# Kernel tuning notes

Hardware: AMD Instinct MI355X
Metric: run time of the kernel (lower is better)

The kernel has to match this reference:

```python
import jax, jax.numpy as jnp
import numpy as np

N_SRC, M, K, H = 100000, 20000, 32, 128
NEG_SLOPE = 0.01  # torch LeakyReLU default


def setup_inputs() -> dict:
    key = jax.random.key(0)
    ks = jax.random.split(key, 8)
    nei = jax.random.randint(ks[0], (M, K), 0, N_SRC)
    h = jax.random.normal(ks[1], (N_SRC, 1), dtype=jnp.float32)
    h_refer = jax.random.normal(ks[2], (M, 1), dtype=jnp.float32)
    # map_l / map_r: Linear(1, H), weight init U[0,1), bias U[0,0.01)
    map_l_w = jax.random.uniform(ks[3], (H, 1), dtype=jnp.float32)
    map_l_b = jax.random.uniform(ks[4], (H,), dtype=jnp.float32) * 0.01
    map_r_w = jax.random.uniform(ks[5], (H, 1), dtype=jnp.float32)
    map_r_b = jax.random.uniform(ks[6], (H,), dtype=jnp.float32) * 0.01
    # att_inter: xavier_normal gain=1.414 on shape (1, 2H)
    std = 1.414 * np.sqrt(2.0 / (1 + 2 * H))
    att_inter = jax.random.normal(ks[7], (1, 2 * H), dtype=jnp.float32) * std
    return {"nei": nei, "h": h, "h_refer": h_refer,
            "map_l_w": map_l_w, "map_l_b": map_l_b,
            "map_r_w": map_r_w, "map_r_b": map_r_b,
            "att_inter": att_inter}


def reference(nei, h, h_refer, map_l_w, map_l_b, map_r_w, map_r_b, att_inter):
    # project scalar features to H dims
    h = jax.nn.relu(h @ map_l_w.T + map_l_b)            # [N, H]
    hr = jax.nn.relu(h_refer @ map_r_w.T + map_r_b)     # [M, H]
    nei_emb = h[nei]                                    # [M, K, H] gather
    # split attention vector to avoid materializing concat([hr, nei_emb])
    a_ref = att_inter[0, :H]                            # [H]
    a_nei = att_inter[0, H:]                            # [H]
    logits = (hr @ a_ref)[:, None] + nei_emb @ a_nei    # [M, K]
    logits = jnp.where(logits >= 0, logits, NEG_SLOPE * logits)  # leakyrelu
    att = jax.nn.softmax(logits, axis=1)                # softmax over neighbors
    lr_inner = jnp.einsum('mkh,mh->mk', nei_emb, hr)    # [M, K]
    out = jax.nn.relu(jnp.sum(att * lr_inner, axis=1, keepdims=True))  # [M, 1]
    return (out, att)
```

## Files before the change

kernel.cpp:

```cpp
#include <hip/hip_runtime.h>

#define N_SRC 100000
#define M_NODES 20000
#define K_NEI 32
#define H_DIM 128
#define NEG_SLOPE 0.01f

#define BLK_M 16
#define SH_STRIDE 132

__global__ __launch_bounds__(128) void intra_att_fused(
    const int*   __restrict__ nei,
    const float* __restrict__ h,
    const float* __restrict__ h_refer,
    const float* __restrict__ map_l_w,
    const float* __restrict__ map_l_b,
    const float* __restrict__ map_r_w,
    const float* __restrict__ map_r_b,
    const float* __restrict__ att_inter,
    float*       __restrict__ out,
    float*       __restrict__ att)
{
    __shared__ float  s_traw[H_DIM];
    __shared__ int    s_ord[H_DIM];
    __shared__ float  s_T[H_DIM];
    __shared__ float  s_wr[H_DIM], s_br[H_DIM], s_ar[H_DIM];
    __shared__ float  s_wl[H_DIM], s_bl[H_DIM];
    __shared__ float  s_cw[H_DIM], s_cb[H_DIM];
    __shared__ float2 s_SA[H_DIM + 1];
    __shared__ float2 s_SH[BLK_M][SH_STRIDE];

    const int tid  = threadIdx.x;
    const int slot = tid >> 3;
    const int u    = tid & 7;
    const int m    = blockIdx.x * BLK_M + slot;

    const int4  nv = *(const int4*)(nei + m * K_NEI + u * 4);
    const float rm = h_refer[m];

    const float wl0 = map_l_w[tid];
    const float bl0 = map_l_b[tid];
    const float t0  = -bl0 / fmaxf(wl0, 1e-30f);
    s_traw[tid] = t0;
    __syncthreads();

    int rank = 0;
    #pragma unroll 8
    for (int i = 0; i < H_DIM; ++i) {
        const float ti = s_traw[i];
        rank += (ti < t0 || (ti == t0 && i < tid)) ? 1 : 0;
    }
    s_ord[rank] = tid;

    const float x0 = h[nv.x], x1 = h[nv.y], x2 = h[nv.z], x3 = h[nv.w];

    __syncthreads();

    const int   src = s_ord[tid];
    const float wls = map_l_w[src];
    const float bls = map_l_b[src];
    const float an  = att_inter[H_DIM + src];
    s_T[tid]  = s_traw[src];
    s_wl[tid] = wls;
    s_bl[tid] = bls;
    s_wr[tid] = map_r_w[src];
    s_br[tid] = map_r_b[src];
    s_ar[tid] = att_inter[src];
    s_cw[tid] = an * wls;
    s_cb[tid] = an * bls;
    __syncthreads();

    if (tid < 8) {
        const int sb = tid * 16;
        float cw[16], cb[16];
        float sw = 0.f, sbv = 0.f;
        #pragma unroll
        for (int i = 0; i < 16; ++i) {
            cw[i] = s_cw[sb + i]; cb[i] = s_cb[sb + i];
            sw += cw[i]; sbv += cb[i];
        }
        float iw = sw, ib = sbv, v;
        v = __shfl_up(iw, 1); if (tid >= 1) iw += v;
        v = __shfl_up(ib, 1); if (tid >= 1) ib += v;
        v = __shfl_up(iw, 2); if (tid >= 2) iw += v;
        v = __shfl_up(ib, 2); if (tid >= 2) ib += v;
        v = __shfl_up(iw, 4); if (tid >= 4) iw += v;
        v = __shfl_up(ib, 4); if (tid >= 4) ib += v;
        float rw = iw - sw, rb = ib - sbv;
        #pragma unroll
        for (int i = 0; i < 16; ++i) {
            s_SA[sb + i] = make_float2(rw, rb);
            rw += cw[i]; rb += cb[i];
        }
        if (tid == 7) s_SA[H_DIM] = make_float2(rw, rb);
    }

    const int sb = u * 16;
    float hrdot = 0.f;
    float cw[16], cb[16];
    float sw = 0.f, sbv = 0.f;
    #pragma unroll
    for (int q = 0; q < 4; ++q) {
        const float4 wr4 = *(const float4*)(s_wr + sb + q * 4);
        const float4 br4 = *(const float4*)(s_br + sb + q * 4);
        const float4 ar4 = *(const float4*)(s_ar + sb + q * 4);
        const float4 wl4 = *(const float4*)(s_wl + sb + q * 4);
        const float4 bl4 = *(const float4*)(s_bl + sb + q * 4);
        const float h0 = fmaxf(0.f, fmaf(rm, wr4.x, br4.x));
        const float h1 = fmaxf(0.f, fmaf(rm, wr4.y, br4.y));
        const float h2 = fmaxf(0.f, fmaf(rm, wr4.z, br4.z));
        const float h3 = fmaxf(0.f, fmaf(rm, wr4.w, br4.w));
        hrdot += h0*ar4.x + h1*ar4.y + h2*ar4.z + h3*ar4.w;
        cw[q*4+0] = h0*wl4.x; cb[q*4+0] = h0*bl4.x;
        cw[q*4+1] = h1*wl4.y; cb[q*4+1] = h1*bl4.y;
        cw[q*4+2] = h2*wl4.z; cb[q*4+2] = h2*bl4.z;
        cw[q*4+3] = h3*wl4.w; cb[q*4+3] = h3*bl4.w;
        sw  += cw[q*4+0] + cw[q*4+1] + cw[q*4+2] + cw[q*4+3];
        sbv += cb[q*4+0] + cb[q*4+1] + cb[q*4+2] + cb[q*4+3];
    }
    {
        float iw = sw, ib = sbv, v;
        v = __shfl_up(iw, 1); if (u >= 1) iw += v;
        v = __shfl_up(ib, 1); if (u >= 1) ib += v;
        v = __shfl_up(iw, 2); if (u >= 2) iw += v;
        v = __shfl_up(ib, 2); if (u >= 2) ib += v;
        v = __shfl_up(iw, 4); if (u >= 4) iw += v;
        v = __shfl_up(ib, 4); if (u >= 4) ib += v;
        float rw = iw - sw, rb = ib - sbv;
        #pragma unroll
        for (int q = 0; q < 8; ++q) {
            float4 t4;
            t4.x = rw; t4.y = rb; rw += cw[q*2];   rb += cb[q*2];
            t4.z = rw; t4.w = rb; rw += cw[q*2+1]; rb += cb[q*2+1];
            *(float4*)(&s_SH[slot][sb + q*2]) = t4;
        }
        if (u == 7) s_SH[slot][H_DIM] = make_float2(rw, rb);
    }
    hrdot += __shfl_xor(hrdot, 1);
    hrdot += __shfl_xor(hrdot, 2);
    hrdot += __shfl_xor(hrdot, 4);

    __syncthreads();

    const float xs[4] = {x0, x1, x2, x3};
    float lg[4], in_[4];
    float mx = -3.4e38f;
    #pragma unroll
    for (int t = 0; t < 4; ++t) {
        const float x = xs[t];
        int r = (s_T[63] < x) ? 64 : 0;
        if (s_T[r+31] < x) r += 32;
        if (s_T[r+15] < x) r += 16;
        if (s_T[r+7]  < x) r += 8;
        if (s_T[r+3]  < x) r += 4;
        if (s_T[r+1]  < x) r += 2;
        if (s_T[r]    < x) r += 1;
        if (s_T[r]    < x) r += 1;
        const float2 sa = s_SA[r];
        const float2 sh = s_SH[slot][r];
        const float l = fmaf(sa.x, x, sa.y) + hrdot;
        lg[t]  = (l >= 0.f) ? l : NEG_SLOPE * l;
        in_[t] = fmaf(sh.x, x, sh.y);
        mx = fmaxf(mx, lg[t]);
    }
    mx = fmaxf(mx, __shfl_xor(mx, 1));
    mx = fmaxf(mx, __shfl_xor(mx, 2));
    mx = fmaxf(mx, __shfl_xor(mx, 4));

    float e[4];
    float se = 0.f, sei = 0.f;
    #pragma unroll
    for (int t = 0; t < 4; ++t) {
        e[t] = __expf(lg[t] - mx);
        se  += e[t];
        sei += e[t] * in_[t];
    }
    se  += __shfl_xor(se, 1);  se  += __shfl_xor(se, 2);  se  += __shfl_xor(se, 4);
    sei += __shfl_xor(sei, 1); sei += __shfl_xor(sei, 2); sei += __shfl_xor(sei, 4);

    const float inv = 1.0f / se;
    const float4 a4 = make_float4(e[0]*inv, e[1]*inv, e[2]*inv, e[3]*inv);
    *(float4*)(att + m * K_NEI + u * 4) = a4;
    if (u == 0) out[m] = fmaxf(0.f, sei * inv);
}

extern "C" void kernel_launch(void* const* d_in, const int* in_sizes, int n_in,
                              void* d_out, int out_size, void* d_ws, size_t ws_size,
                              hipStream_t stream) {
    const int*   nei       = (const int*)  d_in[0];
    const float* h         = (const float*)d_in[1];
    const float* h_refer   = (const float*)d_in[2];
    const float* map_l_w   = (const float*)d_in[3];
    const float* map_l_b   = (const float*)d_in[4];
    const float* map_r_w   = (const float*)d_in[5];
    const float* map_r_b   = (const float*)d_in[6];
    const float* att_inter = (const float*)d_in[7];

    float* out = (float*)d_out;
    float* att = out + M_NODES;

    const int blocks = M_NODES / BLK_M;
    intra_att_fused<<<blocks, 128, 0, stream>>>(
        nei, h, h_refer, map_l_w, map_l_b, map_r_w, map_r_b, att_inter,
        out, att);
}
```

Before: 16.79 us.

## Enlarge blocks to 80 rows and replace binary search with register bucket scan

Blocks now hold 80 nodes with 640 threads, so the per-block sort of the 128 thresholds and the prefix-sum setup are shared across five times as many rows and run 250 times instead of 1250. Only the first 128 threads do the setup work. The dependent shared-memory binary search is replaced by comparing against 16 bucket boundaries held in registers, followed by a short three-step refinement. The sentinel padding in s_T keeps the refinement in bounds. In exchange, 512 threads sit idle during the serial setup, and the extra registers may reduce occupancy. The grid also shrinks to 250 blocks, which could underfill the GPU.

Result: slower. 17.61 us (+4.9%).

```diff
diff --git a/kernel.cpp b/kernel.cpp
--- a/kernel.cpp
+++ b/kernel.cpp
@@ -6,10 +6,11 @@
 #define H_DIM 128
 #define NEG_SLOPE 0.01f
 
-#define BLK_M 16
+#define BLK_M 80
+#define NTHR 640
 #define SH_STRIDE 132
 
-__global__ __launch_bounds__(128) void intra_att_fused(
+__global__ __launch_bounds__(NTHR) void intra_att_fused(
     const int*   __restrict__ nei,
     const float* __restrict__ h,
     const float* __restrict__ h_refer,
@@ -23,7 +24,7 @@
 {
     __shared__ float  s_traw[H_DIM];
     __shared__ int    s_ord[H_DIM];
-    __shared__ float  s_T[H_DIM];
+    __shared__ float  s_T[H_DIM + 8];
     __shared__ float  s_wr[H_DIM], s_br[H_DIM], s_ar[H_DIM];
     __shared__ float  s_wl[H_DIM], s_bl[H_DIM];
     __shared__ float  s_cw[H_DIM], s_cb[H_DIM];
@@ -38,46 +39,52 @@
     const int4  nv = *(const int4*)(nei + m * K_NEI + u * 4);
     const float rm = h_refer[m];
 
-    const float wl0 = map_l_w[tid];
-    const float bl0 = map_l_b[tid];
-    const float t0  = -bl0 / fmaxf(wl0, 1e-30f);
-    s_traw[tid] = t0;
-    __syncthreads();
-
-    int rank = 0;
-    #pragma unroll 8
-    for (int i = 0; i < H_DIM; ++i) {
-        const float ti = s_traw[i];
-        rank += (ti < t0 || (ti == t0 && i < tid)) ? 1 : 0;
-    }
-    s_ord[rank] = tid;
-
+    if (tid < H_DIM) {
+        const float wl0 = map_l_w[tid];
+        const float bl0 = map_l_b[tid];
+        s_traw[tid] = -bl0 / fmaxf(wl0, 1e-30f);
+    }
     const float x0 = h[nv.x], x1 = h[nv.y], x2 = h[nv.z], x3 = h[nv.w];
-
-    __syncthreads();
-
-    const int   src = s_ord[tid];
-    const float wls = map_l_w[src];
-    const float bls = map_l_b[src];
-    const float an  = att_inter[H_DIM + src];
-    s_T[tid]  = s_traw[src];
-    s_wl[tid] = wls;
-    s_bl[tid] = bls;
-    s_wr[tid] = map_r_w[src];
-    s_br[tid] = map_r_b[src];
-    s_ar[tid] = att_inter[src];
-    s_cw[tid] = an * wls;
-    s_cb[tid] = an * bls;
+    __syncthreads();
+
+    if (tid < H_DIM) {
+        const float t0 = s_traw[tid];
+        int rank = 0;
+        #pragma unroll 8
+        for (int i = 0; i < H_DIM; ++i) {
+            const float ti = s_traw[i];
+            rank += (ti < t0 || (ti == t0 && i < tid)) ? 1 : 0;
+        }
+        s_ord[rank] = tid;
+    }
+    __syncthreads();
+
+    if (tid < H_DIM) {
+        const int   src = s_ord[tid];
+        const float wls = map_l_w[src];
+        const float bls = map_l_b[src];
+        const float an  = att_inter[H_DIM + src];
+        s_T[tid]  = s_traw[src];
+        s_wl[tid] = wls;
+        s_bl[tid] = bls;
+        s_wr[tid] = map_r_w[src];
+        s_br[tid] = map_r_b[src];
+        s_ar[tid] = att_inter[src];
+        s_cw[tid] = an * wls;
+        s_cb[tid] = an * bls;
+    } else if (tid < H_DIM + 8) {
+        s_T[tid] = 3.4e38f;
+    }
     __syncthreads();
 
     if (tid < 8) {
-        const int sb = tid * 16;
-        float cw[16], cb[16];
+        const int sb0 = tid * 16;
+        float cwv[16], cbv[16];
         float sw = 0.f, sbv = 0.f;
         #pragma unroll
         for (int i = 0; i < 16; ++i) {
-            cw[i] = s_cw[sb + i]; cb[i] = s_cb[sb + i];
-            sw += cw[i]; sbv += cb[i];
+            cwv[i] = s_cw[sb0 + i]; cbv[i] = s_cb[sb0 + i];
+            sw += cwv[i]; sbv += cbv[i];
         }
         float iw = sw, ib = sbv, v;
         v = __shfl_up(iw, 1); if (tid >= 1) iw += v;
@@ -89,11 +96,15 @@
         float rw = iw - sw, rb = ib - sbv;
         #pragma unroll
         for (int i = 0; i < 16; ++i) {
-            s_SA[sb + i] = make_float2(rw, rb);
-            rw += cw[i]; rb += cb[i];
+            s_SA[sb0 + i] = make_float2(rw, rb);
+            rw += cwv[i]; rb += cbv[i];
         }
         if (tid == 7) s_SA[H_DIM] = make_float2(rw, rb);
     }
+
+    float Tm[16];
+    #pragma unroll
+    for (int i = 0; i < 16; ++i) Tm[i] = s_T[i * 8 + 7];
 
     const int sb = u * 16;
     float hrdot = 0.f;
@@ -148,14 +159,12 @@
     #pragma unroll
     for (int t = 0; t < 4; ++t) {
         const float x = xs[t];
-        int r = (s_T[63] < x) ? 64 : 0;
-        if (s_T[r+31] < x) r += 32;
-        if (s_T[r+15] < x) r += 16;
-        if (s_T[r+7]  < x) r += 8;
-        if (s_T[r+3]  < x) r += 4;
-        if (s_T[r+1]  < x) r += 2;
-        if (s_T[r]    < x) r += 1;
-        if (s_T[r]    < x) r += 1;
+        int r = 0;
+        #pragma unroll
+        for (int i = 0; i < 16; ++i) r += (Tm[i] < x) ? 8 : 0;
+        if (s_T[r + 3] < x) r += 4;
+        if (s_T[r + 1] < x) r += 2;
+        if (s_T[r]     < x) r += 1;
         const float2 sa = s_SA[r];
         const float2 sh = s_SH[slot][r];
         const float l = fmaf(sa.x, x, sa.y) + hrdot;
@@ -200,7 +209,7 @@
     float* att = out + M_NODES;
 
     const int blocks = M_NODES / BLK_M;
-    intra_att_fused<<<blocks, 128, 0, stream>>>(
+    intra_att_fused<<<blocks, NTHR, 0, stream>>>(
         nei, h, h_refer, map_l_w, map_l_b, map_r_w, map_r_b, att_inter,
         out, att);
 }
```
